# Optimization experiments

Hardware: AMD Instinct MI355X
Metric: run time of the kernel (lower is better)

## Reference

```python
import jax, jax.numpy as jnp
import numpy as np
import math

D_MODEL = 1024
N_HEADS = 16
SEQ = 1024
BATCH = 4


def setup_inputs() -> dict:
    key = jax.random.key(0)
    ks = jax.random.split(key, 13)
    s = 1.0 / math.sqrt(D_MODEL)  # keep logits in a sane range
    return {
        "x": jax.random.normal(ks[0], (BATCH, SEQ, D_MODEL), jnp.float32),
        "Wq": jax.random.normal(ks[1], (D_MODEL, D_MODEL), jnp.float32) * s,
        "bq": jnp.zeros((D_MODEL,), jnp.float32),
        "Wk": jax.random.normal(ks[2], (D_MODEL, D_MODEL), jnp.float32) * s,
        "bk": jnp.zeros((D_MODEL,), jnp.float32),
        "Wv": jax.random.normal(ks[3], (D_MODEL, D_MODEL), jnp.float32) * s,
        "bv": jnp.zeros((D_MODEL,), jnp.float32),
        "Wo": jax.random.normal(ks[4], (D_MODEL, D_MODEL), jnp.float32) * s,
        "bo": jnp.zeros((D_MODEL,), jnp.float32),
        "Wimp": jax.random.normal(ks[5], (N_HEADS, D_MODEL), jnp.float32) * s,
        "bimp": jnp.zeros((N_HEADS,), jnp.float32),
        "k_ema": jax.random.normal(ks[6], (SEQ, D_MODEL), jnp.float32),
        "v_ema": jax.random.normal(ks[7], (SEQ, D_MODEL), jnp.float32),
    }


def reference(x, Wq, bq, Wk, bk, Wv, bv, Wo, bo, Wimp, bimp, k_ema, v_ema):
    B, S, D = x.shape
    H = Wimp.shape[0]
    hd = D // H

    def proj(W, b):
        # [B,S,D] -> [B,H,S,hd]
        return (x @ W.T + b).reshape(B, S, H, hd).transpose(0, 2, 1, 3)

    q = proj(Wq, bq)
    k = proj(Wk, bk)
    v = proj(Wv, bv)

    scores = jnp.einsum("bhqd,bhkd->bhqk", q, k) / math.sqrt(hd)

    # importance bias: outer-sum of per-head key/value importance vectors
    k_imp = (k_ema[:S] @ Wimp.T + bimp).T  # [H, S]
    v_imp = (v_ema[:S] @ Wimp.T + bimp).T  # [H, S]
    bias = 0.5 * (k_imp[:, :, None] + v_imp[:, None, :])  # [H, S, S]
    scores = scores + 0.1 * bias[None]

    # causal mask (torch masks before bias add; -inf + finite == -inf, so equivalent)
    causal = jnp.triu(jnp.ones((S, S), bool), k=1)
    scores = jnp.where(causal, -jnp.inf, scores)

    attn = jax.nn.softmax(scores, axis=-1)
    out = jnp.einsum("bhqk,bhkd->bhqd", attn, v)
    out = out.transpose(0, 2, 1, 3).reshape(B, S, D)
    return out @ Wo.T + bo
```

## Files before the change

kernel.cpp:

```cpp
#include <hip/hip_runtime.h>
#include <hip/hip_bf16.h>
#include <math.h>

#define D_MODEL 1024
#define SEQ     1024
#define BATCH   4
#define NHEADS  16
#define HD      64

#define QSC 0.18033688f
#define BSC 0.072134752f

typedef __bf16 bf16x8 __attribute__((ext_vector_type(8)));
typedef __bf16 bf16x4 __attribute__((ext_vector_type(4)));
typedef float  f32x4  __attribute__((ext_vector_type(4)));

__device__ __forceinline__ f32x4 mfma16(bf16x8 a, bf16x8 b, f32x4 c) {
  return __builtin_amdgcn_mfma_f32_16x16x32_bf16(a, b, c, 0, 0, 0);
}

__device__ __forceinline__ void async16(__bf16* lds, const __bf16* g) {
  __builtin_amdgcn_global_load_lds(g, lds, 16, 0, 0);
}

__device__ __forceinline__ float fexp2(float x) {
  float r;
  asm volatile("v_exp_f32 %0, %1" : "=v"(r) : "v"(x));
  return r;
}

__global__ __launch_bounds__(256) void prep_kernel(
    const float* __restrict__ x,
    const float* __restrict__ Wq, const float* __restrict__ Wk,
    const float* __restrict__ Wv, const float* __restrict__ Wo,
    const float* __restrict__ v_ema,
    const float* __restrict__ Wimp, const float* __restrict__ bimp,
    __bf16* __restrict__ x_bf, __bf16* __restrict__ wq_bf, __bf16* __restrict__ wk_bf,
    __bf16* __restrict__ wv_bf, __bf16* __restrict__ wo_bf,
    float* __restrict__ vimp) {
  const int bid = blockIdx.x;
  const int tid = threadIdx.x;
  if (bid < 4096) {
    int i = bid * 256 + tid;
    float4 v = ((const float4*)x)[i];
    bf16x4 o; o[0] = (__bf16)v.x; o[1] = (__bf16)v.y; o[2] = (__bf16)v.z; o[3] = (__bf16)v.w;
    ((bf16x4*)x_bf)[i] = o;
  } else if (bid < 8192) {
    int i = (bid - 4096) * 256 + tid;
    int sel = i >> 18;
    int j = i & 262143;
    const float* s = (sel == 0) ? Wq : (sel == 1) ? Wk : (sel == 2) ? Wv : Wo;
    __bf16* d      = (sel == 0) ? wq_bf : (sel == 1) ? wk_bf : (sel == 2) ? wv_bf : wo_bf;
    float4 v = ((const float4*)s)[j];
    bf16x4 o; o[0] = (__bf16)v.x; o[1] = (__bf16)v.y; o[2] = (__bf16)v.z; o[3] = (__bf16)v.w;
    ((bf16x4*)d)[j] = o;
  } else {
    const int s    = (bid - 8192) * 4 + (tid >> 6);
    const int lane = tid & 63;
    const float4* ve = (const float4*)(v_ema + (size_t)s * D_MODEL);
    float acc0 = 0.f, acc1 = 0.f, acc2 = 0.f, acc3 = 0.f;
    float acc4 = 0.f, acc5 = 0.f, acc6 = 0.f, acc7 = 0.f;
    float acc8 = 0.f, acc9 = 0.f, accA = 0.f, accB = 0.f;
    float accC = 0.f, accD = 0.f, accE = 0.f, accF = 0.f;
    #pragma unroll
    for (int i = 0; i < 4; i++) {
      const int c = lane + i * 64;
      float4 v = ve[c];
      #define VIMP_H(H, ACC)                                                     \
        {                                                                        \
          float4 w = ((const float4*)(Wimp + (H) * D_MODEL))[c];                 \
          ACC += v.x * w.x + v.y * w.y + v.z * w.z + v.w * w.w;                  \
        }
      VIMP_H(0, acc0)  VIMP_H(1, acc1)  VIMP_H(2, acc2)  VIMP_H(3, acc3)
      VIMP_H(4, acc4)  VIMP_H(5, acc5)  VIMP_H(6, acc6)  VIMP_H(7, acc7)
      VIMP_H(8, acc8)  VIMP_H(9, acc9)  VIMP_H(10, accA) VIMP_H(11, accB)
      VIMP_H(12, accC) VIMP_H(13, accD) VIMP_H(14, accE) VIMP_H(15, accF)
      #undef VIMP_H
    }
    #define VIMP_RED(ACC)                                                        \
      for (int mm = 32; mm >= 1; mm >>= 1) ACC += __shfl_xor(ACC, mm);
    VIMP_RED(acc0) VIMP_RED(acc1) VIMP_RED(acc2) VIMP_RED(acc3)
    VIMP_RED(acc4) VIMP_RED(acc5) VIMP_RED(acc6) VIMP_RED(acc7)
    VIMP_RED(acc8) VIMP_RED(acc9) VIMP_RED(accA) VIMP_RED(accB)
    VIMP_RED(accC) VIMP_RED(accD) VIMP_RED(accE) VIMP_RED(accF)
    #undef VIMP_RED
    if (lane == 0) {
      vimp[0  * SEQ + s] = acc0 + bimp[0];  vimp[1  * SEQ + s] = acc1 + bimp[1];
      vimp[2  * SEQ + s] = acc2 + bimp[2];  vimp[3  * SEQ + s] = acc3 + bimp[3];
      vimp[4  * SEQ + s] = acc4 + bimp[4];  vimp[5  * SEQ + s] = acc5 + bimp[5];
      vimp[6  * SEQ + s] = acc6 + bimp[6];  vimp[7  * SEQ + s] = acc7 + bimp[7];
      vimp[8  * SEQ + s] = acc8 + bimp[8];  vimp[9  * SEQ + s] = acc9 + bimp[9];
      vimp[10 * SEQ + s] = accA + bimp[10]; vimp[11 * SEQ + s] = accB + bimp[11];
      vimp[12 * SEQ + s] = accC + bimp[12]; vimp[13 * SEQ + s] = accD + bimp[13];
      vimp[14 * SEQ + s] = accE + bimp[14]; vimp[15 * SEQ + s] = accF + bimp[15];
    }
  }
}

template<bool OUT_BF16>
__global__ __launch_bounds__(256) void gemm_bt(
    const __bf16* __restrict__ A,
    const __bf16* __restrict__ W0, const __bf16* __restrict__ W1, const __bf16* __restrict__ W2,
    const float* __restrict__ b0, const float* __restrict__ b1, const float* __restrict__ b2,
    void* out0, void* out1, void* out2, float sc0, float sc1, float sc2) {
  const int id = blockIdx.x + (blockIdx.y << 3) + (blockIdx.z << 8);
  const int xcd = id & 7;
  const int bx = (id >> 3) & 7;
  const int tt = id >> 6;
  const int z = tt >> 2;
  const int by = (tt & 3) * 8 + xcd;

  const __bf16* W   = (z == 0) ? W0 : (z == 1) ? W1 : W2;
  const float* bias = (z == 0) ? b0 : (z == 1) ? b1 : b2;
  void* out         = (z == 0) ? out0 : (z == 1) ? out1 : out2;
  const float sc    = (z == 0) ? sc0 : (z == 1) ? sc1 : sc2;

  __shared__ __bf16 As[2 * 8192];
  __shared__ __bf16 Bs[2 * 8192];

  const int tid = threadIdx.x;
  const int w = tid >> 6, l = tid & 63;
  const int quad = l >> 4, l16 = l & 15;
  const int wy = w >> 1, wx = w & 1;
  const int row0 = by * 128;
  const int col0 = bx * 128;

  const f32x4 fzero = {0.f, 0.f, 0.f, 0.f};
  f32x4 acc[4][4];
  for (int i = 0; i < 4; i++)
    for (int j = 0; j < 4; j++) acc[i][j] = fzero;

  const int rk = tid >> 3;
  const int csw = (((tid & 7) ^ (rk & 7)) * 8);
  const int tid8 = tid * 8;
  const __bf16* aS = A + (size_t)(row0 + rk) * D_MODEL + csw;
  const __bf16* bS = W + (size_t)(col0 + rk) * D_MODEL + csw;

  const int pch0 = ((0 * 4 + quad) ^ (l16 & 7)) * 8;
  const int pch1 = ((1 * 4 + quad) ^ (l16 & 7)) * 8;

  #pragma unroll
  for (int p = 0; p < 4; ++p) {
    async16(&As[p * 2048 + tid8], aS + (size_t)p * 32 * D_MODEL);
    async16(&Bs[p * 2048 + tid8], bS + (size_t)p * 32 * D_MODEL);
  }

  #pragma unroll 2
  for (int t = 0; t < 16; ++t) {
    const int rb = (t & 1) << 13;
    if (t < 15) {
      const int sb = ((t + 1) & 1) << 13;
      const size_t kk = (size_t)(t + 1) * 64;
      #pragma unroll
      for (int p = 0; p < 4; ++p) {
        async16(&As[sb + p * 2048 + tid8], aS + (size_t)p * 32 * D_MODEL + kk);
        async16(&Bs[sb + p * 2048 + tid8], bS + (size_t)p * 32 * D_MODEL + kk);
      }
      asm volatile("s_waitcnt vmcnt(8)" ::: "memory");
    } else {
      asm volatile("s_waitcnt vmcnt(0)" ::: "memory");
    }
    __builtin_amdgcn_s_barrier();
    #pragma unroll
    for (int ks = 0; ks < 2; ++ks) {
      const int pch = ks ? pch1 : pch0;
      bf16x8 af[4], bfr[4];
      #pragma unroll
      for (int mi = 0; mi < 4; mi++) af[mi]  = *(const bf16x8*)&As[rb + (wy * 64 + mi * 16 + l16) * 64 + pch];
      #pragma unroll
      for (int ni = 0; ni < 4; ni++) bfr[ni] = *(const bf16x8*)&Bs[rb + (wx * 64 + ni * 16 + l16) * 64 + pch];
      if (z == 1) {
        #pragma unroll
        for (int mi = 0; mi < 4; mi++)
          #pragma unroll
          for (int ni = 0; ni < 4; ni++)
            acc[mi][ni] = mfma16(bfr[ni], af[mi], acc[mi][ni]);
      } else {
        #pragma unroll
        for (int mi = 0; mi < 4; mi++)
          #pragma unroll
          for (int ni = 0; ni < 4; ni++)
            acc[mi][ni] = mfma16(af[mi], bfr[ni], acc[mi][ni]);
      }
    }
    __builtin_amdgcn_s_barrier();
  }

  if (z == 1 && OUT_BF16) {
    __bf16* kp = (__bf16*)out;
    #pragma unroll
    for (int ni = 0; ni < 4; ni++) {
      const int wcolbase = col0 + wx * 64 + ni * 16 + quad * 4;
      const float4 b4 = *(const float4*)&bias[wcolbase];
      const float bb[4] = {b4.x, b4.y, b4.z, b4.w};
      #pragma unroll
      for (int mi = 0; mi < 4; mi++) {
        const int token = row0 + wy * 64 + mi * 16 + l16;
        const int bh = (token >> 10) * 16 + (wcolbase >> 6);
        const int colp = ((wcolbase & 63) + ((token & 7) << 3)) & 63;
        union { __bf16 hh[4]; uint2 uu; } pk;
        #pragma unroll
        for (int r = 0; r < 4; r++) pk.hh[r] = (__bf16)(acc[mi][ni][r] + bb[r]);
        *(uint2*)(kp + ((size_t)bh * SEQ + (token & 1023)) * HD + colp) = pk.uu;
      }
    }
  } else if (z == 2 && OUT_BF16) {
    __bf16* vp = (__bf16*)out;
    #pragma unroll
    for (int ni = 0; ni < 4; ni++) {
      const int col = col0 + wx * 64 + ni * 16 + l16;
      const float bv = bias[col];
      #pragma unroll
      for (int mi = 0; mi < 4; mi++) {
        const int token = row0 + wy * 64 + mi * 16 + quad * 4;
        const int bh = (token >> 10) * 16 + (col >> 6);
        const int chk = (token >> 6) & 15;
        const int keyp = ((token & 63) + ((col & 7) << 3)) & 63;
        const size_t base = (((size_t)bh * 16 + chk) * 64 + (col & 63)) * 64 + keyp;
        union { __bf16 hh[4]; uint2 uu; } pk;
        #pragma unroll
        for (int r = 0; r < 4; r++) pk.hh[r] = (__bf16)(acc[mi][ni][r] + bv);
        *(uint2*)(vp + base) = pk.uu;
      }
    }
  } else {
    #pragma unroll
    for (int ni = 0; ni < 4; ni++) {
      const int col = col0 + wx * 64 + ni * 16 + l16;
      const float bv = bias[col];
      #pragma unroll
      for (int mi = 0; mi < 4; mi++) {
        const int row = row0 + wy * 64 + mi * 16 + quad * 4;
        #pragma unroll
        for (int r = 0; r < 4; r++) {
          float v = (acc[mi][ni][r] + bv) * sc;
          if (OUT_BF16) ((__bf16*)out)[(size_t)(row + r) * D_MODEL + col] = (__bf16)v;
          else          ((float*)out)[(size_t)(row + r) * D_MODEL + col] = v;
        }
      }
    }
  }
}

__global__ __launch_bounds__(256) void gemm_o(
    const __bf16* __restrict__ A, const __bf16* __restrict__ W,
    const float* __restrict__ bias, float* __restrict__ out) {
  const int id = blockIdx.x + (blockIdx.y << 4);
  const int xcd = id & 7;
  const int j = id >> 3;
  const int by = (j & 3) * 8 + xcd;
  const int bx = j >> 2;

  __shared__ __bf16 As[2 * 8192];
  __shared__ __bf16 Bs[2 * 4096];

  const int tid = threadIdx.x;
  const int w = tid >> 6, l = tid & 63;
  const int quad = l >> 4, l16 = l & 15;
  const int wy = w >> 1, wx = w & 1;
  const int row0 = by * 128;
  const int col0 = bx * 64;

  const f32x4 fzero = {0.f, 0.f, 0.f, 0.f};
  f32x4 acc[4][2];
  for (int i = 0; i < 4; i++)
    for (int jj = 0; jj < 2; jj++) acc[i][jj] = fzero;

  const int rk = tid >> 3;
  const int csw = (((tid & 7) ^ (rk & 7)) * 8);
  const int tid8 = tid * 8;
  const __bf16* aS = A + (size_t)(row0 + rk) * D_MODEL + csw;
  const __bf16* bS = W + (size_t)(col0 + rk) * D_MODEL + csw;

  const int pch0 = ((0 * 4 + quad) ^ (l16 & 7)) * 8;
  const int pch1 = ((1 * 4 + quad) ^ (l16 & 7)) * 8;

  #pragma unroll
  for (int p = 0; p < 4; ++p)
    async16(&As[p * 2048 + tid8], aS + (size_t)p * 32 * D_MODEL);
  #pragma unroll
  for (int p = 0; p < 2; ++p)
    async16(&Bs[p * 2048 + tid8], bS + (size_t)p * 32 * D_MODEL);

  #pragma unroll 2
  for (int t = 0; t < 16; ++t) {
    const int rbA = (t & 1) << 13;
    const int rbB = (t & 1) << 12;
    if (t < 15) {
      const int sbA = ((t + 1) & 1) << 13;
      const int sbB = ((t + 1) & 1) << 12;
      const size_t kk = (size_t)(t + 1) * 64;
      #pragma unroll
      for (int p = 0; p < 4; ++p)
        async16(&As[sbA + p * 2048 + tid8], aS + (size_t)p * 32 * D_MODEL + kk);
      #pragma unroll
      for (int p = 0; p < 2; ++p)
        async16(&Bs[sbB + p * 2048 + tid8], bS + (size_t)p * 32 * D_MODEL + kk);
      asm volatile("s_waitcnt vmcnt(6)" ::: "memory");
    } else {
      asm volatile("s_waitcnt vmcnt(0)" ::: "memory");
    }
    __builtin_amdgcn_s_barrier();
    #pragma unroll
    for (int ks = 0; ks < 2; ++ks) {
      const int pch = ks ? pch1 : pch0;
      bf16x8 af[4], bfr[2];
      #pragma unroll
      for (int mi = 0; mi < 4; mi++) af[mi]  = *(const bf16x8*)&As[rbA + (wy * 64 + mi * 16 + l16) * 64 + pch];
      #pragma unroll
      for (int ni = 0; ni < 2; ni++) bfr[ni] = *(const bf16x8*)&Bs[rbB + (wx * 32 + ni * 16 + l16) * 64 + pch];
      #pragma unroll
      for (int mi = 0; mi < 4; mi++)
        #pragma unroll
        for (int ni = 0; ni < 2; ni++)
          acc[mi][ni] = mfma16(af[mi], bfr[ni], acc[mi][ni]);
    }
    __builtin_amdgcn_s_barrier();
  }

  #pragma unroll
  for (int ni = 0; ni < 2; ni++) {
    const int col = col0 + wx * 32 + ni * 16 + l16;
    const float bv = bias[col];
    #pragma unroll
    for (int mi = 0; mi < 4; mi++) {
      const int row = row0 + wy * 64 + mi * 16 + quad * 4;
      #pragma unroll
      for (int r = 0; r < 4; r++)
        out[(size_t)(row + r) * D_MODEL + col] = acc[mi][ni][r] + bv;
    }
  }
}

__global__ __launch_bounds__(256, 2) void attn_kernel(
    const __bf16* __restrict__ Qb, const __bf16* __restrict__ Kp,
    const __bf16* __restrict__ Vp, const float* __restrict__ vimp,
    __bf16* __restrict__ Ob) {
  const int id = blockIdx.x;
  const int bh = id & 63;
  const int gg = id >> 6;
  const int b = bh >> 4, h = bh & 15;
  const int tid = threadIdx.x;
  const int wave = tid >> 6, lane = tid & 63;
  const int quad = lane >> 4, l16 = lane & 15;

  __shared__ __bf16 Kl[3][4096];
  __shared__ __bf16 Vl[3][4096];
  __shared__ __bf16 Ps[4][16][72];

  const __bf16* kbase = Kp + (size_t)bh * (SEQ * HD);
  const __bf16* vbase = Vp + (size_t)bh * (SEQ * HD);
  const float* vimpH = vimp + h * SEQ;

  const int rot0 = ((quad + (l16 & 7)) & 7) * 8;
  const int rot1 = ((quad + 4 + (l16 & 7)) & 7) * 8;
  const int frow = l16 * 64;

  const int g0 = gg, g1 = 15 - gg;

  const int qrow0 = g0 * 64 + wave * 16 + l16;
  const int qrow1 = g1 * 64 + wave * 16 + l16;
  const __bf16* qp0 = Qb + (size_t)(b * SEQ + qrow0) * D_MODEL + h * HD;
  const __bf16* qp1 = Qb + (size_t)(b * SEQ + qrow1) * D_MODEL + h * HD;
  bf16x8 qA0 = *(const bf16x8*)(qp0 + quad * 8);
  bf16x8 qA1 = *(const bf16x8*)(qp0 + 32 + quad * 8);
  bf16x8 qB0 = *(const bf16x8*)(qp1 + quad * 8);
  bf16x8 qB1 = *(const bf16x8*)(qp1 + 32 + quad * 8);

  async16(&Kl[0][tid * 8], kbase + tid * 8);
  async16(&Kl[0][2048 + tid * 8], kbase + 2048 + tid * 8);
  async16(&Vl[0][tid * 8], vbase + tid * 8);
  async16(&Vl[0][2048 + tid * 8], vbase + 2048 + tid * 8);
  async16(&Kl[1][tid * 8], kbase + 4096 + tid * 8);
  async16(&Kl[1][2048 + tid * 8], kbase + 4096 + 2048 + tid * 8);
  async16(&Vl[1][tid * 8], vbase + 4096 + tid * 8);
  async16(&Vl[1][2048 + tid * 8], vbase + 4096 + 2048 + tid * 8);

  float l0 = 0.f, l1 = 0.f;
  f32x4 o0[4], o1[4];
  #pragma unroll
  for (int td = 0; td < 4; td++) {
    o0[td][0] = 0.f; o0[td][1] = 0.f; o0[td][2] = 0.f; o0[td][3] = 0.f;
    o1[td][0] = 0.f; o1[td][1] = 0.f; o1[td][2] = 0.f; o1[td][3] = 0.f;
  }

  #pragma unroll 1
  for (int c = 0; c <= g1; ++c) {
    const int buf = c % 3;
    if (c < g1) asm volatile("s_waitcnt vmcnt(4)" ::: "memory");
    else        asm volatile("s_waitcnt vmcnt(0)" ::: "memory");
    __builtin_amdgcn_s_barrier();
    const int kc = c * 64;
    float4 vi[4];
    #pragma unroll
    for (int t = 0; t < 4; t++) vi[t] = *(const float4*)(vimpH + kc + t * 16 + quad * 4);
    __builtin_amdgcn_sched_barrier(0);
    if (c + 2 <= g1) {
      const int nb = (c + 2) % 3;
      const __bf16* gk = kbase + (size_t)(c + 2) * 4096;
      const __bf16* gv = vbase + (size_t)(c + 2) * 4096;
      async16(&Kl[nb][tid * 8], gk + tid * 8);
      async16(&Kl[nb][2048 + tid * 8], gk + 2048 + tid * 8);
      async16(&Vl[nb][tid * 8], gv + tid * 8);
      async16(&Vl[nb][2048 + tid * 8], gv + 2048 + tid * 8);
    }
    __builtin_amdgcn_sched_barrier(0);

    bf16x8 kf0[4], kf1[4], vfr0[4], vfr1[4];
    #pragma unroll
    for (int t = 0; t < 4; t++) {
      kf0[t] = *(const bf16x8*)&Kl[buf][t * 1024 + frow + rot0];
      kf1[t] = *(const bf16x8*)&Kl[buf][t * 1024 + frow + rot1];
    }
    #pragma unroll
    for (int td = 0; td < 4; td++) {
      vfr0[td] = *(const bf16x8*)&Vl[buf][td * 1024 + frow + rot0];
      vfr1[td] = *(const bf16x8*)&Vl[buf][td * 1024 + frow + rot1];
    }
    const f32x4 fz = {0.f, 0.f, 0.f, 0.f};

    {
      f32x4 sacc[4];
      __builtin_amdgcn_s_setprio(1);
      #pragma unroll
      for (int t = 0; t < 4; t++) {
        sacc[t] = mfma16(kf0[t], qB0, fz);
        sacc[t] = mfma16(kf1[t], qB1, sacc[t]);
      }
      __builtin_amdgcn_s_setprio(0);
      float p[4][4];
      float lsum = 0.f;
      #pragma unroll
      for (int t = 0; t < 4; t++) {
        const float vib[4] = {vi[t].x, vi[t].y, vi[t].z, vi[t].w};
        if (c == g1) {
          #pragma unroll
          for (int r = 0; r < 4; r++) {
            float pp = fexp2(sacc[t][r] + BSC * vib[r]);
            pp = (kc + t * 16 + quad * 4 + r <= qrow1) ? pp : 0.f;
            p[t][r] = pp;
            lsum += pp;
          }
        } else {
          #pragma unroll
          for (int r = 0; r < 4; r++) {
            float pp = fexp2(sacc[t][r] + BSC * vib[r]);
            p[t][r] = pp;
            lsum += pp;
          }
        }
      }
      l1 += lsum;
      #pragma unroll
      for (int t = 0; t < 4; t++) {
        union { __bf16 hh[4]; uint2 uu; } pk;
        #pragma unroll
        for (int r = 0; r < 4; r++) pk.hh[r] = (__bf16)p[t][r];
        *(uint2*)&Ps[wave][l16][t * 16 + quad * 4] = pk.uu;
      }
      bf16x8 pf0 = *(const bf16x8*)&Ps[wave][l16][quad * 8];
      bf16x8 pf1 = *(const bf16x8*)&Ps[wave][l16][32 + quad * 8];
      __builtin_amdgcn_s_setprio(1);
      #pragma unroll
      for (int td = 0; td < 4; td++) {
        o1[td] = mfma16(vfr0[td], pf0, o1[td]);
        o1[td] = mfma16(vfr1[td], pf1, o1[td]);
      }
      __builtin_amdgcn_s_setprio(0);
    }

    if (c <= g0) {
      f32x4 sacc[4];
      __builtin_amdgcn_s_setprio(1);
      #pragma unroll
      for (int t = 0; t < 4; t++) {
        sacc[t] = mfma16(kf0[t], qA0, fz);
        sacc[t] = mfma16(kf1[t], qA1, sacc[t]);
      }
      __builtin_amdgcn_s_setprio(0);
      float p[4][4];
      float lsum = 0.f;
      #pragma unroll
      for (int t = 0; t < 4; t++) {
        const float vib[4] = {vi[t].x, vi[t].y, vi[t].z, vi[t].w};
        if (c == g0) {
          #pragma unroll
          for (int r = 0; r < 4; r++) {
            float pp = fexp2(sacc[t][r] + BSC * vib[r]);
            pp = (kc + t * 16 + quad * 4 + r <= qrow0) ? pp : 0.f;
            p[t][r] = pp;
            lsum += pp;
          }
        } else {
          #pragma unroll
          for (int r = 0; r < 4; r++) {
            float pp = fexp2(sacc[t][r] + BSC * vib[r]);
            p[t][r] = pp;
            lsum += pp;
          }
        }
      }
      l0 += lsum;
      #pragma unroll
      for (int t = 0; t < 4; t++) {
        union { __bf16 hh[4]; uint2 uu; } pk;
        #pragma unroll
        for (int r = 0; r < 4; r++) pk.hh[r] = (__bf16)p[t][r];
        *(uint2*)&Ps[wave][l16][t * 16 + quad * 4] = pk.uu;
      }
      bf16x8 pf0 = *(const bf16x8*)&Ps[wave][l16][quad * 8];
      bf16x8 pf1 = *(const bf16x8*)&Ps[wave][l16][32 + quad * 8];
      __builtin_amdgcn_s_setprio(1);
      #pragma unroll
      for (int td = 0; td < 4; td++) {
        o0[td] = mfma16(vfr0[td], pf0, o0[td]);
        o0[td] = mfma16(vfr1[td], pf1, o0[td]);
      }
      __builtin_amdgcn_s_setprio(0);
      if (c == g0) {
        float L = l0;
        L += __shfl_xor(L, 16);
        L += __shfl_xor(L, 32);
        const float il = 1.0f / L;
        __bf16* op = Ob + (size_t)(b * SEQ + qrow0) * D_MODEL + h * HD;
        #pragma unroll
        for (int td = 0; td < 4; td++) {
          union { __bf16 hh[4]; uint2 uu; } pk;
          #pragma unroll
          for (int r = 0; r < 4; r++) pk.hh[r] = (__bf16)(o0[td][r] * il);
          *(uint2*)(op + td * 16 + quad * 4) = pk.uu;
        }
      }
    }
  }

  float L = l1;
  L += __shfl_xor(L, 16);
  L += __shfl_xor(L, 32);
  const float il = 1.0f / L;
  __bf16* op = Ob + (size_t)(b * SEQ + qrow1) * D_MODEL + h * HD;
  #pragma unroll
  for (int td = 0; td < 4; td++) {
    union { __bf16 hh[4]; uint2 uu; } pk;
    #pragma unroll
    for (int r = 0; r < 4; r++) pk.hh[r] = (__bf16)(o1[td][r] * il);
    *(uint2*)(op + td * 16 + quad * 4) = pk.uu;
  }
}

extern "C" void kernel_launch(void* const* d_in, const int* in_sizes, int n_in,
                              void* d_out, int out_size, void* d_ws, size_t ws_size,
                              hipStream_t stream) {
  const float* x     = (const float*)d_in[0];
  const float* Wq    = (const float*)d_in[1];
  const float* bq    = (const float*)d_in[2];
  const float* Wk    = (const float*)d_in[3];
  const float* bk    = (const float*)d_in[4];
  const float* Wv    = (const float*)d_in[5];
  const float* bv    = (const float*)d_in[6];
  const float* Wo    = (const float*)d_in[7];
  const float* bo    = (const float*)d_in[8];
  const float* Wimp  = (const float*)d_in[9];
  const float* bimp  = (const float*)d_in[10];
  const float* v_ema = (const float*)d_in[12];
  float* out = (float*)d_out;

  char* ws = (char*)d_ws;
  __bf16* x_bf  = (__bf16*)(ws);
  __bf16* wq_bf = (__bf16*)(ws + (8ull  << 20));
  __bf16* wk_bf = (__bf16*)(ws + (10ull << 20));
  __bf16* wv_bf = (__bf16*)(ws + (12ull << 20));
  __bf16* wo_bf = (__bf16*)(ws + (14ull << 20));
  __bf16* q_bf  = (__bf16*)(ws + (16ull << 20));
  __bf16* kp_bf = (__bf16*)(ws + (24ull << 20));
  __bf16* vp_bf = (__bf16*)(ws + (32ull << 20));
  __bf16* a_bf  = (__bf16*)(ws + (40ull << 20));
  float*  vimp  = (float*)(ws + (48ull << 20));

  prep_kernel<<<8448, 256, 0, stream>>>(
      x, Wq, Wk, Wv, Wo, v_ema, Wimp, bimp,
      x_bf, wq_bf, wk_bf, wv_bf, wo_bf, vimp);

  gemm_bt<true><<<dim3(8, 32, 3), 256, 0, stream>>>(
      x_bf, wq_bf, wk_bf, wv_bf, bq, bk, bv,
      (void*)q_bf, (void*)kp_bf, (void*)vp_bf, QSC, 1.0f, 1.0f);

  attn_kernel<<<dim3(512), 256, 0, stream>>>(
      q_bf, kp_bf, vp_bf, vimp, a_bf);

  gemm_o<<<dim3(16, 32), 256, 0, stream>>>(a_bf, wo_bf, bo, out);
}
```

Before: 191.7 us.

## Fuse Q/K/V projections into one GEMM sharing the activation tile

Replaces the z-indexed triple GEMM (768 blocks of 128x128 tiles) with a fused kernel in which each block computes a 128x64 tile of Q, K and V together. The x tile is loaded into LDS once and reused across the three weight matrices, cutting redundant activation traffic, and the per-block branch on z goes away. In exchange each block holds 24 accumulator fragments and uses more LDS, which may lower occupancy, and the grid shrinks to 512 blocks.

```diff
diff --git a/kernel.cpp b/kernel.cpp
--- a/kernel.cpp
+++ b/kernel.cpp
@@ -97,66 +97,73 @@
   }
 }
 
-template<bool OUT_BF16>
-__global__ __launch_bounds__(256) void gemm_bt(
+__global__ __launch_bounds__(256) void gemm_qkv(
     const __bf16* __restrict__ A,
-    const __bf16* __restrict__ W0, const __bf16* __restrict__ W1, const __bf16* __restrict__ W2,
-    const float* __restrict__ b0, const float* __restrict__ b1, const float* __restrict__ b2,
-    void* out0, void* out1, void* out2, float sc0, float sc1, float sc2) {
-  const int id = blockIdx.x + (blockIdx.y << 3) + (blockIdx.z << 8);
+    const __bf16* __restrict__ Wq, const __bf16* __restrict__ Wk, const __bf16* __restrict__ Wv,
+    const float* __restrict__ bq, const float* __restrict__ bk, const float* __restrict__ bv,
+    __bf16* __restrict__ qo, __bf16* __restrict__ kp, __bf16* __restrict__ vp) {
+  const int id = blockIdx.x + (blockIdx.y << 4);
   const int xcd = id & 7;
-  const int bx = (id >> 3) & 7;
-  const int tt = id >> 6;
-  const int z = tt >> 2;
-  const int by = (tt & 3) * 8 + xcd;
-
-  const __bf16* W   = (z == 0) ? W0 : (z == 1) ? W1 : W2;
-  const float* bias = (z == 0) ? b0 : (z == 1) ? b1 : b2;
-  void* out         = (z == 0) ? out0 : (z == 1) ? out1 : out2;
-  const float sc    = (z == 0) ? sc0 : (z == 1) ? sc1 : sc2;
+  const int j = id >> 3;
+  const int by = (j & 3) * 8 + xcd;
+  const int bx = j >> 2;
 
   __shared__ __bf16 As[2 * 8192];
-  __shared__ __bf16 Bs[2 * 8192];
+  __shared__ __bf16 Ws[3][2 * 4096];
 
   const int tid = threadIdx.x;
   const int w = tid >> 6, l = tid & 63;
   const int quad = l >> 4, l16 = l & 15;
   const int wy = w >> 1, wx = w & 1;
   const int row0 = by * 128;
-  const int col0 = bx * 128;
+  const int col0 = bx * 64;
 
   const f32x4 fzero = {0.f, 0.f, 0.f, 0.f};
-  f32x4 acc[4][4];
+  f32x4 aq[4][2], ak[4][2], av[4][2];
+  #pragma unroll
   for (int i = 0; i < 4; i++)
-    for (int j = 0; j < 4; j++) acc[i][j] = fzero;
+    #pragma unroll
+    for (int jj = 0; jj < 2; jj++) { aq[i][jj] = fzero; ak[i][jj] = fzero; av[i][jj] = fzero; }
 
   const int rk = tid >> 3;
   const int csw = (((tid & 7) ^ (rk & 7)) * 8);
   const int tid8 = tid * 8;
-  const __bf16* aS = A + (size_t)(row0 + rk) * D_MODEL + csw;
-  const __bf16* bS = W + (size_t)(col0 + rk) * D_MODEL + csw;
+  const __bf16* aS = A  + (size_t)(row0 + rk) * D_MODEL + csw;
+  const __bf16* qS = Wq + (size_t)(col0 + rk) * D_MODEL + csw;
+  const __bf16* kS = Wk + (size_t)(col0 + rk) * D_MODEL + csw;
+  const __bf16* vS = Wv + (size_t)(col0 + rk) * D_MODEL + csw;
 
   const int pch0 = ((0 * 4 + quad) ^ (l16 & 7)) * 8;
   const int pch1 = ((1 * 4 + quad) ^ (l16 & 7)) * 8;
 
   #pragma unroll
-  for (int p = 0; p < 4; ++p) {
+  for (int p = 0; p < 4; ++p)
     async16(&As[p * 2048 + tid8], aS + (size_t)p * 32 * D_MODEL);
-    async16(&Bs[p * 2048 + tid8], bS + (size_t)p * 32 * D_MODEL);
+  #pragma unroll
+  for (int p = 0; p < 2; ++p) {
+    async16(&Ws[0][p * 2048 + tid8], qS + (size_t)p * 32 * D_MODEL);
+    async16(&Ws[1][p * 2048 + tid8], kS + (size_t)p * 32 * D_MODEL);
+    async16(&Ws[2][p * 2048 + tid8], vS + (size_t)p * 32 * D_MODEL);
   }
 
   #pragma unroll 2
   for (int t = 0; t < 16; ++t) {
-    const int rb = (t & 1) << 13;
+    const int rbA = (t & 1) << 13;
+    const int rbW = (t & 1) << 12;
     if (t < 15) {
-      const int sb = ((t + 1) & 1) << 13;
+      const int sbA = ((t + 1) & 1) << 13;
+      const int sbW = ((t + 1) & 1) << 12;
       const size_t kk = (size_t)(t + 1) * 64;
       #pragma unroll
-      for (int p = 0; p < 4; ++p) {
-        async16(&As[sb + p * 2048 + tid8], aS + (size_t)p * 32 * D_MODEL + kk);
-        async16(&Bs[sb + p * 2048 + tid8], bS + (size_t)p * 32 * D_MODEL + kk);
-      }
-      asm volatile("s_waitcnt vmcnt(8)" ::: "memory");
+      for (int p = 0; p < 4; ++p)
+        async16(&As[sbA + p * 2048 + tid8], aS + (size_t)p * 32 * D_MODEL + kk);
+      #pragma unroll
+      for (int p = 0; p < 2; ++p) {
+        async16(&Ws[0][sbW + p * 2048 + tid8], qS + (size_t)p * 32 * D_MODEL + kk);
+        async16(&Ws[1][sbW + p * 2048 + tid8], kS + (size_t)p * 32 * D_MODEL + kk);
+        async16(&Ws[2][sbW + p * 2048 + tid8], vS + (size_t)p * 32 * D_MODEL + kk);
+      }
+      asm volatile("s_waitcnt vmcnt(10)" ::: "memory");
     } else {
       asm volatile("s_waitcnt vmcnt(0)" ::: "memory");
     }
@@ -164,80 +171,72 @@
     #pragma unroll
     for (int ks = 0; ks < 2; ++ks) {
       const int pch = ks ? pch1 : pch0;
-      bf16x8 af[4], bfr[4];
-      #pragma unroll
-      for (int mi = 0; mi < 4; mi++) af[mi]  = *(const bf16x8*)&As[rb + (wy * 64 + mi * 16 + l16) * 64 + pch];
-      #pragma unroll
-      for (int ni = 0; ni < 4; ni++) bfr[ni] = *(const bf16x8*)&Bs[rb + (wx * 64 + ni * 16 + l16) * 64 + pch];
-      if (z == 1) {
+      bf16x8 af[4], qf[2], kf[2], vf[2];
+      #pragma unroll
+      for (int mi = 0; mi < 4; mi++)
+        af[mi] = *(const bf16x8*)&As[rbA + (wy * 64 + mi * 16 + l16) * 64 + pch];
+      #pragma unroll
+      for (int ni = 0; ni < 2; ni++) {
+        const int wrow = (wx * 32 + ni * 16 + l16) * 64 + pch;
+        qf[ni] = *(const bf16x8*)&Ws[0][rbW + wrow];
+        kf[ni] = *(const bf16x8*)&Ws[1][rbW + wrow];
+        vf[ni] = *(const bf16x8*)&Ws[2][rbW + wrow];
+      }
+      #pragma unroll
+      for (int mi = 0; mi < 4; mi++)
         #pragma unroll
-        for (int mi = 0; mi < 4; mi++)
-          #pragma unroll
-          for (int ni = 0; ni < 4; ni++)
-            acc[mi][ni] = mfma16(bfr[ni], af[mi], acc[mi][ni]);
-      } else {
-        #pragma unroll
-        for (int mi = 0; mi < 4; mi++)
-          #pragma unroll
-          for (int ni = 0; ni < 4; ni++)
-            acc[mi][ni] = mfma16(af[mi], bfr[ni], acc[mi][ni]);
-      }
+        for (int ni = 0; ni < 2; ni++) {
+          aq[mi][ni] = mfma16(af[mi], qf[ni], aq[mi][ni]);
+          ak[mi][ni] = mfma16(kf[ni], af[mi], ak[mi][ni]);
+          av[mi][ni] = mfma16(af[mi], vf[ni], av[mi][ni]);
+        }
     }
     __builtin_amdgcn_s_barrier();
   }
 
-  if (z == 1 && OUT_BF16) {
-    __bf16* kp = (__bf16*)out;
-    #pragma unroll
-    for (int ni = 0; ni < 4; ni++) {
-      const int wcolbase = col0 + wx * 64 + ni * 16 + quad * 4;
-      const float4 b4 = *(const float4*)&bias[wcolbase];
-      const float bb[4] = {b4.x, b4.y, b4.z, b4.w};
-      #pragma unroll
-      for (int mi = 0; mi < 4; mi++) {
-        const int token = row0 + wy * 64 + mi * 16 + l16;
-        const int bh = (token >> 10) * 16 + (wcolbase >> 6);
-        const int colp = ((wcolbase & 63) + ((token & 7) << 3)) & 63;
-        union { __bf16 hh[4]; uint2 uu; } pk;
-        #pragma unroll
-        for (int r = 0; r < 4; r++) pk.hh[r] = (__bf16)(acc[mi][ni][r] + bb[r]);
-        *(uint2*)(kp + ((size_t)bh * SEQ + (token & 1023)) * HD + colp) = pk.uu;
-      }
-    }
-  } else if (z == 2 && OUT_BF16) {
-    __bf16* vp = (__bf16*)out;
-    #pragma unroll
-    for (int ni = 0; ni < 4; ni++) {
-      const int col = col0 + wx * 64 + ni * 16 + l16;
-      const float bv = bias[col];
-      #pragma unroll
-      for (int mi = 0; mi < 4; mi++) {
-        const int token = row0 + wy * 64 + mi * 16 + quad * 4;
-        const int bh = (token >> 10) * 16 + (col >> 6);
-        const int chk = (token >> 6) & 15;
-        const int keyp = ((token & 63) + ((col & 7) << 3)) & 63;
-        const size_t base = (((size_t)bh * 16 + chk) * 64 + (col & 63)) * 64 + keyp;
-        union { __bf16 hh[4]; uint2 uu; } pk;
-        #pragma unroll
-        for (int r = 0; r < 4; r++) pk.hh[r] = (__bf16)(acc[mi][ni][r] + bv);
-        *(uint2*)(vp + base) = pk.uu;
-      }
-    }
-  } else {
-    #pragma unroll
-    for (int ni = 0; ni < 4; ni++) {
-      const int col = col0 + wx * 64 + ni * 16 + l16;
-      const float bv = bias[col];
-      #pragma unroll
-      for (int mi = 0; mi < 4; mi++) {
-        const int row = row0 + wy * 64 + mi * 16 + quad * 4;
-        #pragma unroll
-        for (int r = 0; r < 4; r++) {
-          float v = (acc[mi][ni][r] + bv) * sc;
-          if (OUT_BF16) ((__bf16*)out)[(size_t)(row + r) * D_MODEL + col] = (__bf16)v;
-          else          ((float*)out)[(size_t)(row + r) * D_MODEL + col] = v;
-        }
-      }
+  #pragma unroll
+  for (int ni = 0; ni < 2; ni++) {
+    const int col = col0 + wx * 32 + ni * 16 + l16;
+    const float bqv = bq[col];
+    #pragma unroll
+    for (int mi = 0; mi < 4; mi++) {
+      const int row = row0 + wy * 64 + mi * 16 + quad * 4;
+      #pragma unroll
+      for (int r = 0; r < 4; r++)
+        qo[(size_t)(row + r) * D_MODEL + col] = (__bf16)((aq[mi][ni][r] + bqv) * QSC);
+    }
+  }
+  #pragma unroll
+  for (int ni = 0; ni < 2; ni++) {
+    const int wcolbase = col0 + wx * 32 + ni * 16 + quad * 4;
+    const float4 b4 = *(const float4*)&bk[wcolbase];
+    const float bb[4] = {b4.x, b4.y, b4.z, b4.w};
+    #pragma unroll
+    for (int mi = 0; mi < 4; mi++) {
+      const int token = row0 + wy * 64 + mi * 16 + l16;
+      const int bh = (token >> 10) * 16 + (wcolbase >> 6);
+      const int colp = ((wcolbase & 63) + ((token & 7) << 3)) & 63;
+      union { __bf16 hh[4]; uint2 uu; } pk;
+      #pragma unroll
+      for (int r = 0; r < 4; r++) pk.hh[r] = (__bf16)(ak[mi][ni][r] + bb[r]);
+      *(uint2*)(kp + ((size_t)bh * SEQ + (token & 1023)) * HD + colp) = pk.uu;
+    }
+  }
+  #pragma unroll
+  for (int ni = 0; ni < 2; ni++) {
+    const int col = col0 + wx * 32 + ni * 16 + l16;
+    const float bvv = bv[col];
+    #pragma unroll
+    for (int mi = 0; mi < 4; mi++) {
+      const int token = row0 + wy * 64 + mi * 16 + quad * 4;
+      const int bh = (token >> 10) * 16 + (col >> 6);
+      const int chk = (token >> 6) & 15;
+      const int keyp = ((token & 63) + ((col & 7) << 3)) & 63;
+      const size_t base = (((size_t)bh * 16 + chk) * 64 + (col & 63)) * 64 + keyp;
+      union { __bf16 hh[4]; uint2 uu; } pk;
+      #pragma unroll
+      for (int r = 0; r < 4; r++) pk.hh[r] = (__bf16)(av[mi][ni][r] + bvv);
+      *(uint2*)(vp + base) = pk.uu;
     }
   }
 }
@@ -581,9 +580,8 @@
       x, Wq, Wk, Wv, Wo, v_ema, Wimp, bimp,
       x_bf, wq_bf, wk_bf, wv_bf, wo_bf, vimp);
 
-  gemm_bt<true><<<dim3(8, 32, 3), 256, 0, stream>>>(
-      x_bf, wq_bf, wk_bf, wv_bf, bq, bk, bv,
-      (void*)q_bf, (void*)kp_bf, (void*)vp_bf, QSC, 1.0f, 1.0f);
+  gemm_qkv<<<dim3(16, 32), 256, 0, stream>>>(
+      x_bf, wq_bf, wk_bf, wv_bf, bq, bk, bv, q_bf, kp_bf, vp_bf);
 
   attn_kernel<<<dim3(512), 256, 0, stream>>>(
       q_bf, kp_bf, vp_bf, vimp, a_bf);
```

Result: faster. 180.9 us (-5.6%).
